# Kernel tuning notes

Measured on AMD Instinct MI355X. Metric: run time of the kernel, lower is better.

## Reference

```python
import jax, jax.numpy as jnp
import numpy as np

# Problem dims
M, K, N = 16384, 1024, 1024
# QuantParams baked as constants (Python scalars in the original module)
INPUT_SCALE, INPUT_ZP = 0.05, 3
WEIGHT_SCALE, WEIGHT_ZP = 0.02, 0
OUTPUT_SCALE, OUTPUT_ZP = 0.1, -5
QMIN, QMAX = -128, 127
# round(combined_scale * 1024) computed in Python, exactly as in the torch module
SCALE_INT = round(INPUT_SCALE * WEIGHT_SCALE / OUTPUT_SCALE * 1024)  # = 10


def setup_inputs() -> dict:
    key = jax.random.key(0)
    k1, k2, k3 = jax.random.split(key, 3)
    x = jax.random.randint(k1, (M, K), -128, 128, dtype=jnp.int32).astype(jnp.int8)
    weight_int = jax.random.randint(k2, (N, K), -128, 128, dtype=jnp.int32).astype(jnp.int8)
    bias_int = jax.random.randint(k3, (N,), -1000, 1000, dtype=jnp.int32)
    return {"x": x, "weight_int": weight_int, "bias_int": bias_int}


def reference(x, weight_int, bias_int):
    # F.linear(x.int32 - input_zp, W.int32 - weight_zp, bias_int)
    xi = x.astype(jnp.int32) - INPUT_ZP            # [M, K] int32
    wi = weight_int.astype(jnp.int32) - WEIGHT_ZP  # [N, K] int32
    acc = jnp.matmul(xi, wi.T) + bias_int          # [M, N] int32 accumulate
    # integer requant: (acc * scale_int) // 1024 in int64 (torch // is floor div,
    # matching jnp floor_divide semantics)
    res = (acc.astype(jnp.int64) * SCALE_INT) // 1024
    res = jnp.clip(res + OUTPUT_ZP, QMIN, QMAX)
    return res.astype(jnp.int8)
```

## Files before the change

### kernel.cpp

```cpp
#include <hip/hip_runtime.h>
#include <stdint.h>

#define M_DIM 16384
#define N_DIM 1024
#define K_DIM 1024

#define BM 128
#define BN 128
#define BK 64

using i32x4 = __attribute__((ext_vector_type(4))) int;

__device__ __forceinline__ int pack4(int4 v) {
    return (v.x & 0xFF) | ((v.y & 0xFF) << 8) | ((v.z & 0xFF) << 16) | ((v.w & 0xFF) << 24);
}

__global__ __launch_bounds__(256) void pack_x_kernel(const int* __restrict__ x,
                                                     int8_t* __restrict__ xq) {
    const int4* xin = (const int4*)x;
    int* xout = (int*)xq;
    size_t base = (size_t)blockIdx.x * 1024;
    int tid = threadIdx.x;
#pragma unroll
    for (int i = 0; i < 4; ++i) {
        size_t idx = base + (size_t)i * 256 + tid;
        int4 v = xin[idx];
        xout[idx] = pack4(v);
    }
}

__global__ __launch_bounds__(256) void pack_w_corr_kernel(const int* __restrict__ w,
                                                          const int* __restrict__ bias,
                                                          int8_t* __restrict__ wq,
                                                          int* __restrict__ corr) {
    int col = blockIdx.x;
    int t = threadIdx.x;
    int4 v = ((const int4*)(w + (size_t)col * K_DIM))[t];
    ((int*)(wq + (size_t)col * K_DIM))[t] = pack4(v);
    int s = v.x + v.y + v.z + v.w;
#pragma unroll
    for (int m = 1; m < 64; m <<= 1) s += __shfl_xor(s, m);
    __shared__ int partial[4];
    if ((t & 63) == 0) partial[t >> 6] = s;
    __syncthreads();
    if (t == 0) {
        int total = partial[0] + partial[1] + partial[2] + partial[3];
        corr[col] = bias[col] - 3 * total;
    }
}

__global__ __launch_bounds__(256) void gemm_kernel(const int8_t* __restrict__ A,
                                                   const int8_t* __restrict__ B,
                                                   const int* __restrict__ corr,
                                                   int* __restrict__ out) {
    __shared__ int8_t Asm[BM * BK];
    __shared__ int8_t Bsm[BN * BK];

    int bid = blockIdx.x;
    int swz = (bid & 7) * 128 + (bid >> 3);
    int mtile = swz >> 3;
    int ntile = swz & 7;
    int m0 = mtile * BM;
    int n0 = ntile * BN;

    int tid = threadIdx.x;
    int lane = tid & 63;
    int wave = tid >> 6;
    int wm = wave >> 1;
    int wn = wave & 1;

    i32x4 acc[4][4];
#pragma unroll
    for (int i = 0; i < 4; ++i)
#pragma unroll
        for (int j = 0; j < 4; ++j)
            acc[i][j] = (i32x4){0, 0, 0, 0};

    int r16 = lane & 15;
    int krow = lane >> 4;

    for (int kt = 0; kt < K_DIM / BK; ++kt) {
        const int8_t* Ag = A + (size_t)m0 * K_DIM + kt * BK;
        const int8_t* Bg = B + (size_t)n0 * K_DIM + kt * BK;
#pragma unroll
        for (int i = 0; i < 2; ++i) {
            int f = i * 256 + tid;
            int row = f >> 2, ch = f & 3;
            __builtin_amdgcn_global_load_lds(
                (const __attribute__((address_space(1))) unsigned int*)(Ag + (size_t)row * K_DIM + ch * 16),
                (__attribute__((address_space(3))) unsigned int*)(Asm + f * 16),
                16, 0, 0);
        }
#pragma unroll
        for (int i = 0; i < 2; ++i) {
            int f = i * 256 + tid;
            int row = f >> 2, ch = f & 3;
            __builtin_amdgcn_global_load_lds(
                (const __attribute__((address_space(1))) unsigned int*)(Bg + (size_t)row * K_DIM + ch * 16),
                (__attribute__((address_space(3))) unsigned int*)(Bsm + f * 16),
                16, 0, 0);
        }
        __syncthreads();

        i32x4 afr[4], bfr[4];
#pragma unroll
        for (int i = 0; i < 4; ++i) {
            afr[i] = *(const i32x4*)(Asm + (wm * 64 + i * 16 + r16) * BK + krow * 16);
            bfr[i] = *(const i32x4*)(Bsm + (wn * 64 + i * 16 + r16) * BK + krow * 16);
        }
#pragma unroll
        for (int i = 0; i < 4; ++i)
#pragma unroll
            for (int j = 0; j < 4; ++j)
                acc[i][j] = __builtin_amdgcn_mfma_i32_16x16x64_i8(afr[i], bfr[j], acc[i][j], 0, 0, 0);
        __syncthreads();
    }

    int col16 = lane & 15;
    int rbase = (lane >> 4) * 4;
#pragma unroll
    for (int j = 0; j < 4; ++j) {
        int c = n0 + wn * 64 + j * 16 + col16;
        int cr = corr[c];
#pragma unroll
        for (int i = 0; i < 4; ++i) {
            int rrow = m0 + wm * 64 + i * 16 + rbase;
#pragma unroll
            for (int r = 0; r < 4; ++r) {
                int t = acc[i][j][r] + cr;
                int res = ((t * 10) >> 10) - 5;
                res = res < -128 ? -128 : (res > 127 ? 127 : res);
                out[(size_t)(rrow + r) * N_DIM + c] = res;
            }
        }
    }
}

extern "C" void kernel_launch(void* const* d_in, const int* in_sizes, int n_in,
                              void* d_out, int out_size, void* d_ws, size_t ws_size,
                              hipStream_t stream) {
    (void)in_sizes; (void)n_in; (void)out_size; (void)ws_size;
    const int* x    = (const int*)d_in[0];
    const int* w    = (const int*)d_in[1];
    const int* bias = (const int*)d_in[2];
    int* out = (int*)d_out;

    int8_t* xq = (int8_t*)d_ws;
    int8_t* wq = xq + (size_t)M_DIM * K_DIM;
    int* corr  = (int*)(wq + (size_t)N_DIM * K_DIM);

    pack_x_kernel<<<4096, 256, 0, stream>>>(x, xq);
    pack_w_corr_kernel<<<N_DIM, 256, 0, stream>>>(w, bias, wq, corr);
    gemm_kernel<<<(M_DIM / BM) * (N_DIM / BN), 256, 0, stream>>>(xq, wq, corr, out);
}
```

Before: 141.3 us.

## Fuse int8 packing of X into GEMM with register-staged double-buffered LDS

Drops the separate pass that packs int32 X into int8. The GEMM now reads int32 X directly, packs it in registers and writes it into padded LDS tiles. Next-tile global loads are prefetched into registers while the MFMAs run, using double buffering and one barrier per k-step. The tradeoff is that each GEMM block re-reads 4-byte X elements across all 8 N-tiles, so global and L2 traffic for A grows, and register pressure rises.

```diff
diff --git a/kernel.cpp b/kernel.cpp
--- a/kernel.cpp
+++ b/kernel.cpp
@@ -8,25 +8,12 @@
 #define BM 128
 #define BN 128
 #define BK 64
+#define LDSW 20
 
 using i32x4 = __attribute__((ext_vector_type(4))) int;
 
 __device__ __forceinline__ int pack4(int4 v) {
     return (v.x & 0xFF) | ((v.y & 0xFF) << 8) | ((v.z & 0xFF) << 16) | ((v.w & 0xFF) << 24);
-}
-
-__global__ __launch_bounds__(256) void pack_x_kernel(const int* __restrict__ x,
-                                                     int8_t* __restrict__ xq) {
-    const int4* xin = (const int4*)x;
-    int* xout = (int*)xq;
-    size_t base = (size_t)blockIdx.x * 1024;
-    int tid = threadIdx.x;
-#pragma unroll
-    for (int i = 0; i < 4; ++i) {
-        size_t idx = base + (size_t)i * 256 + tid;
-        int4 v = xin[idx];
-        xout[idx] = pack4(v);
-    }
 }
 
 __global__ __launch_bounds__(256) void pack_w_corr_kernel(const int* __restrict__ w,
@@ -49,25 +36,25 @@
     }
 }
 
-__global__ __launch_bounds__(256) void gemm_kernel(const int8_t* __restrict__ A,
-                                                   const int8_t* __restrict__ B,
-                                                   const int* __restrict__ corr,
-                                                   int* __restrict__ out) {
-    __shared__ int8_t Asm[BM * BK];
-    __shared__ int8_t Bsm[BN * BK];
+__global__ __launch_bounds__(256, 2) void gemm_fused_kernel(const int* __restrict__ X,
+                                                            const int8_t* __restrict__ Wq,
+                                                            const int* __restrict__ corr,
+                                                            int* __restrict__ out) {
+    __shared__ int Asm[2][BM * LDSW];
+    __shared__ int Bsm[2][BN * LDSW];
 
     int bid = blockIdx.x;
     int swz = (bid & 7) * 128 + (bid >> 3);
-    int mtile = swz >> 3;
-    int ntile = swz & 7;
-    int m0 = mtile * BM;
-    int n0 = ntile * BN;
+    int m0 = (swz >> 3) * BM;
+    int n0 = (swz & 7) * BN;
 
     int tid = threadIdx.x;
     int lane = tid & 63;
     int wave = tid >> 6;
     int wm = wave >> 1;
     int wn = wave & 1;
+    int r16 = lane & 15;
+    int krow = lane >> 4;
 
     i32x4 acc[4][4];
 #pragma unroll
@@ -76,44 +63,53 @@
         for (int j = 0; j < 4; ++j)
             acc[i][j] = (i32x4){0, 0, 0, 0};
 
-    int r16 = lane & 15;
-    int krow = lane >> 4;
+    int arow = tid >> 4;
+    int adcol = tid & 15;
+    const int* Abase = X + (size_t)(m0 + arow) * K_DIM + adcol * 4;
+    int brow = tid >> 2;
+    int bdc4 = tid & 3;
+    const int8_t* Bbase = Wq + (size_t)(n0 + brow) * K_DIM + bdc4 * 16;
+
+    int4 areg[8];
+    int4 breg[2];
+
+#define LOAD_TILE(kt)                                                              \
+    {                                                                              \
+        _Pragma("unroll") for (int i = 0; i < 8; ++i)                              \
+            areg[i] = *(const int4*)(Abase + (size_t)i * 16 * K_DIM + (kt) * BK);  \
+        _Pragma("unroll") for (int i = 0; i < 2; ++i)                              \
+            breg[i] = *(const int4*)(Bbase + (size_t)i * 64 * K_DIM + (kt) * BK);  \
+    }
+
+#define WRITE_TILE(buf)                                                            \
+    {                                                                              \
+        _Pragma("unroll") for (int i = 0; i < 8; ++i)                              \
+            Asm[buf][(i * 16 + arow) * LDSW + adcol] = pack4(areg[i]);             \
+        _Pragma("unroll") for (int i = 0; i < 2; ++i)                              \
+            *(int4*)&Bsm[buf][(i * 64 + brow) * LDSW + bdc4 * 4] = breg[i];        \
+    }
+
+    LOAD_TILE(0);
+    WRITE_TILE(0);
 
     for (int kt = 0; kt < K_DIM / BK; ++kt) {
-        const int8_t* Ag = A + (size_t)m0 * K_DIM + kt * BK;
-        const int8_t* Bg = B + (size_t)n0 * K_DIM + kt * BK;
-#pragma unroll
-        for (int i = 0; i < 2; ++i) {
-            int f = i * 256 + tid;
-            int row = f >> 2, ch = f & 3;
-            __builtin_amdgcn_global_load_lds(
-                (const __attribute__((address_space(1))) unsigned int*)(Ag + (size_t)row * K_DIM + ch * 16),
-                (__attribute__((address_space(3))) unsigned int*)(Asm + f * 16),
-                16, 0, 0);
-        }
-#pragma unroll
-        for (int i = 0; i < 2; ++i) {
-            int f = i * 256 + tid;
-            int row = f >> 2, ch = f & 3;
-            __builtin_amdgcn_global_load_lds(
-                (const __attribute__((address_space(1))) unsigned int*)(Bg + (size_t)row * K_DIM + ch * 16),
-                (__attribute__((address_space(3))) unsigned int*)(Bsm + f * 16),
-                16, 0, 0);
-        }
+        int cur = kt & 1;
         __syncthreads();
+        if (kt < 15) LOAD_TILE(kt + 1);
 
         i32x4 afr[4], bfr[4];
 #pragma unroll
         for (int i = 0; i < 4; ++i) {
-            afr[i] = *(const i32x4*)(Asm + (wm * 64 + i * 16 + r16) * BK + krow * 16);
-            bfr[i] = *(const i32x4*)(Bsm + (wn * 64 + i * 16 + r16) * BK + krow * 16);
+            afr[i] = *(const i32x4*)&Asm[cur][(wm * 64 + i * 16 + r16) * LDSW + krow * 4];
+            bfr[i] = *(const i32x4*)&Bsm[cur][(wn * 64 + i * 16 + r16) * LDSW + krow * 4];
         }
 #pragma unroll
         for (int i = 0; i < 4; ++i)
 #pragma unroll
             for (int j = 0; j < 4; ++j)
                 acc[i][j] = __builtin_amdgcn_mfma_i32_16x16x64_i8(afr[i], bfr[j], acc[i][j], 0, 0, 0);
-        __syncthreads();
+
+        if (kt < 15) WRITE_TILE(cur ^ 1);
     }
 
     int col16 = lane & 15;
@@ -134,6 +130,8 @@
             }
         }
     }
+#undef LOAD_TILE
+#undef WRITE_TILE
 }
 
 extern "C" void kernel_launch(void* const* d_in, const int* in_sizes, int n_in,
@@ -145,11 +143,9 @@
     const int* bias = (const int*)d_in[2];
     int* out = (int*)d_out;
 
-    int8_t* xq = (int8_t*)d_ws;
-    int8_t* wq = xq + (size_t)M_DIM * K_DIM;
+    int8_t* wq = (int8_t*)d_ws;
     int* corr  = (int*)(wq + (size_t)N_DIM * K_DIM);
 
-    pack_x_kernel<<<4096, 256, 0, stream>>>(x, xq);
     pack_w_corr_kernel<<<N_DIM, 256, 0, stream>>>(w, bias, wq, corr);
-    gemm_kernel<<<(M_DIM / BM) * (N_DIM / BN), 256, 0, stream>>>(xq, wq, corr, out);
+    gemm_fused_kernel<<<(M_DIM / BM) * (N_DIM / BN), 256, 0, stream>>>(x, wq, corr, out);
 }
```

New measurement: 174.6 us. 1.24x slower.

## Pre-tile packed int8 operands with XOR-swizzled LDS layout

Applied to the files above, without the earlier changes.

The pack kernels now write X and W in a tiled layout, with one contiguous BM x BK block per (tile, k-step) and 16-byte chunks XOR-swizzled within each row. The GEMM's global-to-LDS loads become fully contiguous streams, and fragment reads use the swizzled slot to avoid LDS bank conflicts. The pack kernel's input reads become more strided (each thread reads 64 contiguous ints), which could slow the pack stage.

```diff
diff --git a/kernel.cpp b/kernel.cpp
--- a/kernel.cpp
+++ b/kernel.cpp
@@ -8,6 +8,8 @@
 #define BM 128
 #define BN 128
 #define BK 64
+#define NKT (K_DIM / BK)
+#define TILE_BYTES (BM * BK)
 
 using i32x4 = __attribute__((ext_vector_type(4))) int;
 
@@ -15,52 +17,66 @@
     return (v.x & 0xFF) | ((v.y & 0xFF) << 8) | ((v.z & 0xFF) << 16) | ((v.w & 0xFF) << 24);
 }
 
-__global__ __launch_bounds__(256) void pack_x_kernel(const int* __restrict__ x,
-                                                     int8_t* __restrict__ xq) {
-    const int4* xin = (const int4*)x;
-    int* xout = (int*)xq;
-    size_t base = (size_t)blockIdx.x * 1024;
+
+__global__ __launch_bounds__(256) void pack_x_kernel(const int* __restrict__ X,
+                                                     int8_t* __restrict__ xqT) {
+    int mtile = blockIdx.x >> 4;
+    int kt = blockIdx.x & 15;
+    int8_t* outT = xqT + (size_t)blockIdx.x * TILE_BYTES;
     int tid = threadIdx.x;
 #pragma unroll
-    for (int i = 0; i < 4; ++i) {
-        size_t idx = base + (size_t)i * 256 + tid;
-        int4 v = xin[idx];
-        xout[idx] = pack4(v);
+    for (int i = 0; i < 2; ++i) {
+        int c = i * 256 + tid;
+        int row = c >> 2;
+        int sig = c & 3;
+        const int* src = X + ((size_t)(mtile * BM + row)) * K_DIM + kt * BK + sig * 16;
+        int4 p;
+        p.x = pack4(*(const int4*)(src + 0));
+        p.y = pack4(*(const int4*)(src + 4));
+        p.z = pack4(*(const int4*)(src + 8));
+        p.w = pack4(*(const int4*)(src + 12));
+        int s = sig ^ ((row >> 1) & 3);
+        *(int4*)(outT + ((size_t)row * 4 + s) * 16) = p;
     }
 }
 
 __global__ __launch_bounds__(256) void pack_w_corr_kernel(const int* __restrict__ w,
                                                           const int* __restrict__ bias,
-                                                          int8_t* __restrict__ wq,
+                                                          int8_t* __restrict__ wqT,
                                                           int* __restrict__ corr) {
-    int col = blockIdx.x;
+    int n = blockIdx.x;
     int t = threadIdx.x;
-    int4 v = ((const int4*)(w + (size_t)col * K_DIM))[t];
-    ((int*)(wq + (size_t)col * K_DIM))[t] = pack4(v);
-    int s = v.x + v.y + v.z + v.w;
+    int4 v = ((const int4*)(w + (size_t)n * K_DIM))[t];
+    int pk = pack4(v);
+    int kt = t >> 4;
+    int sig = (t >> 2) & 3;
+    int d = t & 3;
+    int rowin = n & 127;
+    int ntile = n >> 7;
+    int s = sig ^ ((rowin >> 1) & 3);
+    ((int*)(wqT + ((size_t)(ntile * NKT + kt)) * TILE_BYTES))[(rowin * 4 + s) * 4 + d] = pk;
+
+    int sum = v.x + v.y + v.z + v.w;
 #pragma unroll
-    for (int m = 1; m < 64; m <<= 1) s += __shfl_xor(s, m);
+    for (int m = 1; m < 64; m <<= 1) sum += __shfl_xor(sum, m);
     __shared__ int partial[4];
-    if ((t & 63) == 0) partial[t >> 6] = s;
+    if ((t & 63) == 0) partial[t >> 6] = sum;
     __syncthreads();
-    if (t == 0) {
-        int total = partial[0] + partial[1] + partial[2] + partial[3];
-        corr[col] = bias[col] - 3 * total;
-    }
+    if (t == 0)
+        corr[n] = bias[n] - 3 * (partial[0] + partial[1] + partial[2] + partial[3]);
 }
 
-__global__ __launch_bounds__(256) void gemm_kernel(const int8_t* __restrict__ A,
-                                                   const int8_t* __restrict__ B,
+__global__ __launch_bounds__(256) void gemm_kernel(const int8_t* __restrict__ xqT,
+                                                   const int8_t* __restrict__ wqT,
                                                    const int* __restrict__ corr,
                                                    int* __restrict__ out) {
-    __shared__ int8_t Asm[BM * BK];
-    __shared__ int8_t Bsm[BN * BK];
+    __shared__ int8_t Asm[TILE_BYTES];
+    __shared__ int8_t Bsm[TILE_BYTES];
 
     int bid = blockIdx.x;
     int swz = (bid & 7) * 128 + (bid >> 3);
     int mtile = swz >> 3;
     int ntile = swz & 7;
-    int m0 = mtile * BM;
     int n0 = ntile * BN;
 
     int tid = threadIdx.x;
@@ -68,6 +84,9 @@
     int wave = tid >> 6;
     int wm = wave >> 1;
     int wn = wave & 1;
+    int r16 = lane & 15;
+    int krow = lane >> 4;
+    int slot = krow ^ ((r16 >> 1) & 3);
 
     i32x4 acc[4][4];
 #pragma unroll
@@ -76,27 +95,25 @@
         for (int j = 0; j < 4; ++j)
             acc[i][j] = (i32x4){0, 0, 0, 0};
 
-    int r16 = lane & 15;
-    int krow = lane >> 4;
+    const int8_t* Abase = xqT + (size_t)mtile * NKT * TILE_BYTES;
+    const int8_t* Bbase = wqT + (size_t)ntile * NKT * TILE_BYTES;
 
-    for (int kt = 0; kt < K_DIM / BK; ++kt) {
-        const int8_t* Ag = A + (size_t)m0 * K_DIM + kt * BK;
-        const int8_t* Bg = B + (size_t)n0 * K_DIM + kt * BK;
+    for (int kt = 0; kt < NKT; ++kt) {
+        const int8_t* Ag = Abase + (size_t)kt * TILE_BYTES;
+        const int8_t* Bg = Bbase + (size_t)kt * TILE_BYTES;
 #pragma unroll
         for (int i = 0; i < 2; ++i) {
             int f = i * 256 + tid;
-            int row = f >> 2, ch = f & 3;
             __builtin_amdgcn_global_load_lds(
-                (const __attribute__((address_space(1))) unsigned int*)(Ag + (size_t)row * K_DIM + ch * 16),
+                (const __attribute__((address_space(1))) unsigned int*)(Ag + (size_t)f * 16),
                 (__attribute__((address_space(3))) unsigned int*)(Asm + f * 16),
                 16, 0, 0);
         }
 #pragma unroll
         for (int i = 0; i < 2; ++i) {
             int f = i * 256 + tid;
-            int row = f >> 2, ch = f & 3;
             __builtin_amdgcn_global_load_lds(
-                (const __attribute__((address_space(1))) unsigned int*)(Bg + (size_t)row * K_DIM + ch * 16),
+                (const __attribute__((address_space(1))) unsigned int*)(Bg + (size_t)f * 16),
                 (__attribute__((address_space(3))) unsigned int*)(Bsm + f * 16),
                 16, 0, 0);
         }
@@ -105,8 +122,8 @@
         i32x4 afr[4], bfr[4];
 #pragma unroll
         for (int i = 0; i < 4; ++i) {
-            afr[i] = *(const i32x4*)(Asm + (wm * 64 + i * 16 + r16) * BK + krow * 16);
-            bfr[i] = *(const i32x4*)(Bsm + (wn * 64 + i * 16 + r16) * BK + krow * 16);
+            afr[i] = *(const i32x4*)(Asm + (size_t)(wm * 64 + i * 16 + r16) * 64 + slot * 16);
+            bfr[i] = *(const i32x4*)(Bsm + (size_t)(wn * 64 + i * 16 + r16) * 64 + slot * 16);
         }
 #pragma unroll
         for (int i = 0; i < 4; ++i)
@@ -116,6 +133,7 @@
         __syncthreads();
     }
 
+    int m0 = mtile * BM;
     int col16 = lane & 15;
     int rbase = (lane >> 4) * 4;
 #pragma unroll
@@ -145,11 +163,11 @@
     const int* bias = (const int*)d_in[2];
     int* out = (int*)d_out;
 
-    int8_t* xq = (int8_t*)d_ws;
-    int8_t* wq = xq + (size_t)M_DIM * K_DIM;
-    int* corr  = (int*)(wq + (size_t)N_DIM * K_DIM);
+    int8_t* xqT = (int8_t*)d_ws;
+    int8_t* wqT = xqT + (size_t)M_DIM * K_DIM;
+    int* corr   = (int*)(wqT + (size_t)N_DIM * K_DIM);
 
-    pack_x_kernel<<<4096, 256, 0, stream>>>(x, xq);
-    pack_w_corr_kernel<<<N_DIM, 256, 0, stream>>>(w, bias, wq, corr);
-    gemm_kernel<<<(M_DIM / BM) * (N_DIM / BN), 256, 0, stream>>>(xq, wq, corr, out);
+    pack_x_kernel<<<(M_DIM / BM) * NKT, 256, 0, stream>>>(x, xqT);
+    pack_w_corr_kernel<<<N_DIM, 256, 0, stream>>>(w, bias, wqT, corr);
+    gemm_kernel<<<(M_DIM / BM) * (N_DIM / BN), 256, 0, stream>>>(xqT, wqT, corr, out);
 }
```

After: 136.4 us. 3.5% less time.
